# Performance work log

Hardware: AMD Instinct MI355X
Metric: run time of the kernel (lower is better)

The kernel has to match this reference:

```python
import jax, jax.numpy as jnp
import numpy as np

EPS = 1e-12  # torch.nn.functional.normalize default eps


def _l2norm(x, axis):
    n = jnp.sqrt(jnp.sum(x * x, axis=axis, keepdims=True))
    return x / jnp.maximum(n, EPS)


def setup_inputs() -> dict:
    key = jax.random.key(0)
    k1, k2 = jax.random.split(key)
    B, n_with_neg, neighbor, n_facet, emb_dim = 4096, 1, 128, 8, 16
    features = jax.random.normal(k1, (B, n_with_neg, n_facet * emb_dim), dtype=jnp.float32)
    metapath_features = jax.random.normal(
        k2, (B, n_with_neg, neighbor, n_facet * emb_dim), dtype=jnp.float32)
    return {
        "features": features,
        "metapath_features": metapath_features,
        "emb_dim": emb_dim,
        "n_facet": n_facet,
        "n_iter": 4,
    }


def reference(features, metapath_features, emb_dim, n_facet, n_iter):
    B, n = features.shape[0], features.shape[1]
    N = metapath_features.shape[2]
    # x: [B, n, F, D], z: [B, n, N, F, D]
    x = features.reshape(B, n, n_facet, emb_dim)
    z = metapath_features.reshape(B, n, N, n_facet, emb_dim)
    x = _l2norm(x, axis=3)
    z = _l2norm(z, axis=4)
    u = x
    for clus_iter in range(n_iter):
        # routing logits: dot over emb_dim -> [B, n, N, F]
        p = jnp.einsum('bnkfd,bnfd->bnkf', z, u)
        p = jax.nn.softmax(p, axis=3)
        # weighted sum over neighbors -> [B, n, F, D]
        u = jnp.einsum('bnkfd,bnkf->bnfd', z, p) + x
        if clus_iter < n_iter - 1:
            u = _l2norm(u, axis=3)
    return u.reshape(B, n_facet * emb_dim)
```

## Files before the change

### kernel.cpp

```cpp
#include <hip/hip_runtime.h>
#include <math.h>


#define CC 128

typedef unsigned u32x2 __attribute__((ext_vector_type(2)));

template<int CTRL>
__device__ __forceinline__ float dpp_add(float x) {
    int y = __builtin_amdgcn_update_dpp(0, __float_as_int(x), CTRL, 0xF, 0xF, true);
    return x + __int_as_float(y);
}
#define DPP_XOR1 0xB1
#define DPP_XOR2 0x4E
#define DPP_HMIR 0x141
#define DPP_MIR  0x140

__device__ __forceinline__ float xor16_add(float v) {
#if __has_builtin(__builtin_amdgcn_permlane16_swap)
    u32x2 r = __builtin_amdgcn_permlane16_swap(__float_as_uint(v), __float_as_uint(v), false, false);
    return __uint_as_float(r.x) + __uint_as_float(r.y);
#else
    return v + __shfl_xor(v, 16);
#endif
}
__device__ __forceinline__ float xor32_add(float v) {
#if __has_builtin(__builtin_amdgcn_permlane32_swap)
    u32x2 r = __builtin_amdgcn_permlane32_swap(__float_as_uint(v), __float_as_uint(v), false, false);
    return __uint_as_float(r.x) + __uint_as_float(r.y);
#else
    return v + __shfl_xor(v, 32);
#endif
}

__device__ __forceinline__ float rsq_guard(float s) {
    return __builtin_amdgcn_rsqf(fmaxf(s, 1e-24f));
}

__global__ __launch_bounds__(256, 4)
void hete_routing_kernel(const float* __restrict__ feat,
                         const float* __restrict__ mp,
                         float* __restrict__ out)
{
    __shared__ float part[2][4][CC];

    const int t = threadIdx.x;
    const int b = blockIdx.x;
    const int wave = t >> 6;
    const int lane = t & 63;
    const int cg = lane & 15;
    const int kgl = lane >> 4;
    const int kg = wave * 4 + kgl;
    const int c0 = cg * 8;

    const float* zg = mp + (size_t)b * (128 * CC);

    float4 za0[8], za1[8];
#pragma unroll
    for (int kk = 0; kk < 8; ++kk) {
        const float* p = zg + (kg * 8 + kk) * CC + c0;
        za0[kk] = *reinterpret_cast<const float4*>(p);
        za1[kk] = *reinterpret_cast<const float4*>(p + 4);
    }
#pragma unroll
    for (int kk = 0; kk < 8; ++kk) {
        float s = za0[kk].x * za0[kk].x + za0[kk].y * za0[kk].y
                + za0[kk].z * za0[kk].z + za0[kk].w * za0[kk].w
                + za1[kk].x * za1[kk].x + za1[kk].y * za1[kk].y
                + za1[kk].z * za1[kk].z + za1[kk].w * za1[kk].w;
        s = dpp_add<DPP_XOR1>(s);
        const float inv = rsq_guard(s);
        za0[kk].x *= inv; za0[kk].y *= inv; za0[kk].z *= inv; za0[kk].w *= inv;
        za1[kk].x *= inv; za1[kk].y *= inv; za1[kk].z *= inv; za1[kk].w *= inv;
    }

    float xr[8], ur[8];
    {
        const float* p = feat + (size_t)b * CC + c0;
        const float4 a = *reinterpret_cast<const float4*>(p);
        const float4 c = *reinterpret_cast<const float4*>(p + 4);
        xr[0] = a.x; xr[1] = a.y; xr[2] = a.z; xr[3] = a.w;
        xr[4] = c.x; xr[5] = c.y; xr[6] = c.z; xr[7] = c.w;
        float s = 0.f;
#pragma unroll
        for (int j = 0; j < 8; ++j) s += xr[j] * xr[j];
        s = dpp_add<DPP_XOR1>(s);
        const float inv = rsq_guard(s);
#pragma unroll
        for (int j = 0; j < 8; ++j) { xr[j] *= inv; ur[j] = xr[j]; }
    }

#pragma unroll
    for (int it = 0; it < 4; ++it) {
        float w[8];
#pragma unroll
        for (int kk = 0; kk < 8; ++kk) {
            float pl = za0[kk].x * ur[0] + za0[kk].y * ur[1]
                     + za0[kk].z * ur[2] + za0[kk].w * ur[3]
                     + za1[kk].x * ur[4] + za1[kk].y * ur[5]
                     + za1[kk].z * ur[6] + za1[kk].w * ur[7];
            w[kk] = dpp_add<DPP_XOR1>(pl);
        }
#pragma unroll
        for (int kk = 0; kk < 8; ++kk) {
            const float e = __expf(w[kk]);
            float su = dpp_add<DPP_XOR2>(e);
            su = dpp_add<DPP_HMIR>(su);
            su = dpp_add<DPP_MIR>(su);
            w[kk] = e * __builtin_amdgcn_rcpf(su);
        }

        float pu[8];
#pragma unroll
        for (int j = 0; j < 8; ++j) pu[j] = 0.f;
#pragma unroll
        for (int kk = 0; kk < 8; ++kk) {
            pu[0] += za0[kk].x * w[kk];
            pu[1] += za0[kk].y * w[kk];
            pu[2] += za0[kk].z * w[kk];
            pu[3] += za0[kk].w * w[kk];
            pu[4] += za1[kk].x * w[kk];
            pu[5] += za1[kk].y * w[kk];
            pu[6] += za1[kk].z * w[kk];
            pu[7] += za1[kk].w * w[kk];
        }
#pragma unroll
        for (int j = 0; j < 8; ++j) {
            pu[j] = xor16_add(pu[j]);
            pu[j] = xor32_add(pu[j]);
        }
        if (kgl == 0) {
            float* dst = &part[it & 1][wave][c0];
            *reinterpret_cast<float4*>(dst)     = make_float4(pu[0], pu[1], pu[2], pu[3]);
            *reinterpret_cast<float4*>(dst + 4) = make_float4(pu[4], pu[5], pu[6], pu[7]);
        }
        __syncthreads();

        float un[8];
#pragma unroll
        for (int j = 0; j < 8; ++j) un[j] = xr[j];
#pragma unroll
        for (int wv = 0; wv < 4; ++wv) {
            const float* src = &part[it & 1][wv][c0];
            const float4 a = *reinterpret_cast<const float4*>(src);
            const float4 c = *reinterpret_cast<const float4*>(src + 4);
            un[0] += a.x; un[1] += a.y; un[2] += a.z; un[3] += a.w;
            un[4] += c.x; un[5] += c.y; un[6] += c.z; un[7] += c.w;
        }

        if (it < 3) {
            float s = 0.f;
#pragma unroll
            for (int j = 0; j < 8; ++j) s += un[j] * un[j];
            s = dpp_add<DPP_XOR1>(s);
            const float inv = rsq_guard(s);
#pragma unroll
            for (int j = 0; j < 8; ++j) ur[j] = un[j] * inv;
        } else if (wave == 0 && kgl == 0) {
            float* dst = out + (size_t)b * CC + c0;
            *reinterpret_cast<float4*>(dst)     = make_float4(un[0], un[1], un[2], un[3]);
            *reinterpret_cast<float4*>(dst + 4) = make_float4(un[4], un[5], un[6], un[7]);
        }
    }
}

extern "C" void kernel_launch(void* const* d_in, const int* in_sizes, int n_in,
                              void* d_out, int out_size, void* d_ws, size_t ws_size,
                              hipStream_t stream) {
    const float* feat = (const float*)d_in[0];
    const float* mp   = (const float*)d_in[1];
    float* out = (float*)d_out;
    const int B = in_sizes[0] / CC;
    hete_routing_kernel<<<B, 256, 0, stream>>>(feat, mp, out);
}
```

Measured before the change: 53.28 us.

## Process eight batches per block with async global-to-LDS prefetch of next batch

Each block now handles eight consecutive batch rows instead of one. While the current row is being computed from registers, the next row's neighbor features (64 KB) stream into shared memory through global_load_lds. Each wave waits only on its own loads before pulling the prefetched tile into registers. This is meant to overlap HBM traffic with the routing math and cut per-block launch overhead, at the cost of 64 KB LDS per block, lower occupancy (launch bounds drop to 2) and a grid of only 512 blocks.

New measurement: 70.61 us. 1.33x slower.

```diff
diff --git a/kernel.cpp b/kernel.cpp
--- a/kernel.cpp
+++ b/kernel.cpp
@@ -3,6 +3,7 @@
 
 
 #define CC 128
+#define NB 8
 
 typedef unsigned u32x2 __attribute__((ext_vector_type(2)));
 
@@ -17,149 +18,182 @@
 #define DPP_MIR  0x140
 
 __device__ __forceinline__ float xor16_add(float v) {
-#if __has_builtin(__builtin_amdgcn_permlane16_swap)
     u32x2 r = __builtin_amdgcn_permlane16_swap(__float_as_uint(v), __float_as_uint(v), false, false);
     return __uint_as_float(r.x) + __uint_as_float(r.y);
-#else
-    return v + __shfl_xor(v, 16);
-#endif
 }
 __device__ __forceinline__ float xor32_add(float v) {
-#if __has_builtin(__builtin_amdgcn_permlane32_swap)
     u32x2 r = __builtin_amdgcn_permlane32_swap(__float_as_uint(v), __float_as_uint(v), false, false);
     return __uint_as_float(r.x) + __uint_as_float(r.y);
-#else
-    return v + __shfl_xor(v, 32);
-#endif
-}
-
+}
 __device__ __forceinline__ float rsq_guard(float s) {
     return __builtin_amdgcn_rsqf(fmaxf(s, 1e-24f));
 }
 
-__global__ __launch_bounds__(256, 4)
+__global__ __launch_bounds__(256, 2)
 void hete_routing_kernel(const float* __restrict__ feat,
                          const float* __restrict__ mp,
                          float* __restrict__ out)
 {
+    __shared__ float zbuf[128 * CC];
     __shared__ float part[2][4][CC];
 
     const int t = threadIdx.x;
-    const int b = blockIdx.x;
     const int wave = t >> 6;
     const int lane = t & 63;
     const int cg = lane & 15;
     const int kgl = lane >> 4;
     const int kg = wave * 4 + kgl;
     const int c0 = cg * 8;
-
-    const float* zg = mp + (size_t)b * (128 * CC);
+    const int b0 = blockIdx.x * NB;
 
     float4 za0[8], za1[8];
-#pragma unroll
-    for (int kk = 0; kk < 8; ++kk) {
-        const float* p = zg + (kg * 8 + kk) * CC + c0;
-        za0[kk] = *reinterpret_cast<const float4*>(p);
-        za1[kk] = *reinterpret_cast<const float4*>(p + 4);
+
+    {
+        const float* zg = mp + (size_t)b0 * (128 * CC);
+#pragma unroll
+        for (int kk = 0; kk < 8; ++kk) {
+            const float* p = zg + (kg * 8 + kk) * CC + c0;
+            za0[kk] = *reinterpret_cast<const float4*>(p);
+            za1[kk] = *reinterpret_cast<const float4*>(p + 4);
+        }
     }
-#pragma unroll
-    for (int kk = 0; kk < 8; ++kk) {
-        float s = za0[kk].x * za0[kk].x + za0[kk].y * za0[kk].y
-                + za0[kk].z * za0[kk].z + za0[kk].w * za0[kk].w
-                + za1[kk].x * za1[kk].x + za1[kk].y * za1[kk].y
-                + za1[kk].z * za1[kk].z + za1[kk].w * za1[kk].w;
-        s = dpp_add<DPP_XOR1>(s);
-        const float inv = rsq_guard(s);
-        za0[kk].x *= inv; za0[kk].y *= inv; za0[kk].z *= inv; za0[kk].w *= inv;
-        za1[kk].x *= inv; za1[kk].y *= inv; za1[kk].z *= inv; za1[kk].w *= inv;
+    {
+        const float* src = mp + (size_t)(b0 + 1) * (128 * CC) + wave * 4096 + lane * 4;
+        float* dst = zbuf + wave * 4096;
+#pragma unroll
+        for (int j = 0; j < 16; ++j) {
+            __builtin_amdgcn_global_load_lds(
+                (const __attribute__((address_space(1))) void*)(src + j * 256),
+                (__attribute__((address_space(3))) void*)(dst + j * 256),
+                16, 0, 0);
+        }
     }
 
-    float xr[8], ur[8];
-    {
-        const float* p = feat + (size_t)b * CC + c0;
-        const float4 a = *reinterpret_cast<const float4*>(p);
-        const float4 c = *reinterpret_cast<const float4*>(p + 4);
-        xr[0] = a.x; xr[1] = a.y; xr[2] = a.z; xr[3] = a.w;
-        xr[4] = c.x; xr[5] = c.y; xr[6] = c.z; xr[7] = c.w;
-        float s = 0.f;
-#pragma unroll
-        for (int j = 0; j < 8; ++j) s += xr[j] * xr[j];
-        s = dpp_add<DPP_XOR1>(s);
-        const float inv = rsq_guard(s);
-#pragma unroll
-        for (int j = 0; j < 8; ++j) { xr[j] *= inv; ur[j] = xr[j]; }
-    }
-
-#pragma unroll
-    for (int it = 0; it < 4; ++it) {
-        float w[8];
+#pragma unroll 1
+    for (int i = 0; i < NB; ++i) {
+        const int b = b0 + i;
+
 #pragma unroll
         for (int kk = 0; kk < 8; ++kk) {
-            float pl = za0[kk].x * ur[0] + za0[kk].y * ur[1]
-                     + za0[kk].z * ur[2] + za0[kk].w * ur[3]
-                     + za1[kk].x * ur[4] + za1[kk].y * ur[5]
-                     + za1[kk].z * ur[6] + za1[kk].w * ur[7];
-            w[kk] = dpp_add<DPP_XOR1>(pl);
-        }
-#pragma unroll
-        for (int kk = 0; kk < 8; ++kk) {
-            const float e = __expf(w[kk]);
-            float su = dpp_add<DPP_XOR2>(e);
-            su = dpp_add<DPP_HMIR>(su);
-            su = dpp_add<DPP_MIR>(su);
-            w[kk] = e * __builtin_amdgcn_rcpf(su);
-        }
-
-        float pu[8];
-#pragma unroll
-        for (int j = 0; j < 8; ++j) pu[j] = 0.f;
-#pragma unroll
-        for (int kk = 0; kk < 8; ++kk) {
-            pu[0] += za0[kk].x * w[kk];
-            pu[1] += za0[kk].y * w[kk];
-            pu[2] += za0[kk].z * w[kk];
-            pu[3] += za0[kk].w * w[kk];
-            pu[4] += za1[kk].x * w[kk];
-            pu[5] += za1[kk].y * w[kk];
-            pu[6] += za1[kk].z * w[kk];
-            pu[7] += za1[kk].w * w[kk];
-        }
-#pragma unroll
-        for (int j = 0; j < 8; ++j) {
-            pu[j] = xor16_add(pu[j]);
-            pu[j] = xor32_add(pu[j]);
-        }
-        if (kgl == 0) {
-            float* dst = &part[it & 1][wave][c0];
-            *reinterpret_cast<float4*>(dst)     = make_float4(pu[0], pu[1], pu[2], pu[3]);
-            *reinterpret_cast<float4*>(dst + 4) = make_float4(pu[4], pu[5], pu[6], pu[7]);
-        }
-        __syncthreads();
-
-        float un[8];
-#pragma unroll
-        for (int j = 0; j < 8; ++j) un[j] = xr[j];
-#pragma unroll
-        for (int wv = 0; wv < 4; ++wv) {
-            const float* src = &part[it & 1][wv][c0];
-            const float4 a = *reinterpret_cast<const float4*>(src);
-            const float4 c = *reinterpret_cast<const float4*>(src + 4);
-            un[0] += a.x; un[1] += a.y; un[2] += a.z; un[3] += a.w;
-            un[4] += c.x; un[5] += c.y; un[6] += c.z; un[7] += c.w;
-        }
-
-        if (it < 3) {
-            float s = 0.f;
-#pragma unroll
-            for (int j = 0; j < 8; ++j) s += un[j] * un[j];
+            float s = za0[kk].x * za0[kk].x + za0[kk].y * za0[kk].y
+                    + za0[kk].z * za0[kk].z + za0[kk].w * za0[kk].w
+                    + za1[kk].x * za1[kk].x + za1[kk].y * za1[kk].y
+                    + za1[kk].z * za1[kk].z + za1[kk].w * za1[kk].w;
             s = dpp_add<DPP_XOR1>(s);
             const float inv = rsq_guard(s);
-#pragma unroll
-            for (int j = 0; j < 8; ++j) ur[j] = un[j] * inv;
-        } else if (wave == 0 && kgl == 0) {
-            float* dst = out + (size_t)b * CC + c0;
-            *reinterpret_cast<float4*>(dst)     = make_float4(un[0], un[1], un[2], un[3]);
-            *reinterpret_cast<float4*>(dst + 4) = make_float4(un[4], un[5], un[6], un[7]);
+            za0[kk].x *= inv; za0[kk].y *= inv; za0[kk].z *= inv; za0[kk].w *= inv;
+            za1[kk].x *= inv; za1[kk].y *= inv; za1[kk].z *= inv; za1[kk].w *= inv;
+        }
+
+        float xr[8], ur[8];
+        {
+            const float* p = feat + (size_t)b * CC + c0;
+            const float4 a = *reinterpret_cast<const float4*>(p);
+            const float4 c = *reinterpret_cast<const float4*>(p + 4);
+            xr[0] = a.x; xr[1] = a.y; xr[2] = a.z; xr[3] = a.w;
+            xr[4] = c.x; xr[5] = c.y; xr[6] = c.z; xr[7] = c.w;
+            float s = 0.f;
+#pragma unroll
+            for (int j = 0; j < 8; ++j) s += xr[j] * xr[j];
+            s = dpp_add<DPP_XOR1>(s);
+            const float inv = rsq_guard(s);
+#pragma unroll
+            for (int j = 0; j < 8; ++j) { xr[j] *= inv; ur[j] = xr[j]; }
+        }
+
+#pragma unroll
+        for (int it = 0; it < 4; ++it) {
+            float w[8];
+#pragma unroll
+            for (int kk = 0; kk < 8; ++kk) {
+                float pl = za0[kk].x * ur[0] + za0[kk].y * ur[1]
+                         + za0[kk].z * ur[2] + za0[kk].w * ur[3]
+                         + za1[kk].x * ur[4] + za1[kk].y * ur[5]
+                         + za1[kk].z * ur[6] + za1[kk].w * ur[7];
+                w[kk] = dpp_add<DPP_XOR1>(pl);
+            }
+#pragma unroll
+            for (int kk = 0; kk < 8; ++kk) {
+                const float e = __expf(w[kk]);
+                float su = dpp_add<DPP_XOR2>(e);
+                su = dpp_add<DPP_HMIR>(su);
+                su = dpp_add<DPP_MIR>(su);
+                w[kk] = e * __builtin_amdgcn_rcpf(su);
+            }
+
+            float pu[8];
+#pragma unroll
+            for (int j = 0; j < 8; ++j) pu[j] = 0.f;
+#pragma unroll
+            for (int kk = 0; kk < 8; ++kk) {
+                pu[0] += za0[kk].x * w[kk];
+                pu[1] += za0[kk].y * w[kk];
+                pu[2] += za0[kk].z * w[kk];
+                pu[3] += za0[kk].w * w[kk];
+                pu[4] += za1[kk].x * w[kk];
+                pu[5] += za1[kk].y * w[kk];
+                pu[6] += za1[kk].z * w[kk];
+                pu[7] += za1[kk].w * w[kk];
+            }
+#pragma unroll
+            for (int j = 0; j < 8; ++j) {
+                pu[j] = xor16_add(pu[j]);
+                pu[j] = xor32_add(pu[j]);
+            }
+            if (kgl == 0) {
+                float* dst = &part[it & 1][wave][c0];
+                *reinterpret_cast<float4*>(dst)     = make_float4(pu[0], pu[1], pu[2], pu[3]);
+                *reinterpret_cast<float4*>(dst + 4) = make_float4(pu[4], pu[5], pu[6], pu[7]);
+            }
+            __syncthreads();
+
+            float un[8];
+#pragma unroll
+            for (int j = 0; j < 8; ++j) un[j] = xr[j];
+#pragma unroll
+            for (int wv = 0; wv < 4; ++wv) {
+                const float* src = &part[it & 1][wv][c0];
+                const float4 a = *reinterpret_cast<const float4*>(src);
+                const float4 c = *reinterpret_cast<const float4*>(src + 4);
+                un[0] += a.x; un[1] += a.y; un[2] += a.z; un[3] += a.w;
+                un[4] += c.x; un[5] += c.y; un[6] += c.z; un[7] += c.w;
+            }
+
+            if (it < 3) {
+                float s = 0.f;
+#pragma unroll
+                for (int j = 0; j < 8; ++j) s += un[j] * un[j];
+                s = dpp_add<DPP_XOR1>(s);
+                const float inv = rsq_guard(s);
+#pragma unroll
+                for (int j = 0; j < 8; ++j) ur[j] = un[j] * inv;
+            } else if (wave == 0 && kgl == 0) {
+                float* dst = out + (size_t)b * CC + c0;
+                *reinterpret_cast<float4*>(dst)     = make_float4(un[0], un[1], un[2], un[3]);
+                *reinterpret_cast<float4*>(dst + 4) = make_float4(un[4], un[5], un[6], un[7]);
+            }
+        }
+
+        if (i + 1 < NB) {
+            asm volatile("s_waitcnt vmcnt(0)" ::: "memory");
+#pragma unroll
+            for (int kk = 0; kk < 8; ++kk) {
+                const float* p = zbuf + (kg * 8 + kk) * CC + c0;
+                za0[kk] = *reinterpret_cast<const float4*>(p);
+                za1[kk] = *reinterpret_cast<const float4*>(p + 4);
+            }
+            asm volatile("s_waitcnt lgkmcnt(0)" ::: "memory");
+            if (i + 2 < NB) {
+                const float* src = mp + (size_t)(b0 + i + 2) * (128 * CC) + wave * 4096 + lane * 4;
+                float* dst = zbuf + wave * 4096;
+#pragma unroll
+                for (int j = 0; j < 16; ++j) {
+                    __builtin_amdgcn_global_load_lds(
+                        (const __attribute__((address_space(1))) void*)(src + j * 256),
+                        (__attribute__((address_space(3))) void*)(dst + j * 256),
+                        16, 0, 0);
+                }
+            }
         }
     }
 }
@@ -171,5 +205,5 @@
     const float* mp   = (const float*)d_in[1];
     float* out = (float*)d_out;
     const int B = in_sizes[0] / CC;
-    hete_routing_kernel<<<B, 256, 0, stream>>>(feat, mp, out);
-}
+    hete_routing_kernel<<<B / NB, 256, 0, stream>>>(feat, mp, out);
+}
```

## Process four batches per block with z prefetch and packed f32x2 math

Applied to the files above, without the earlier changes.

Each block now handles four consecutive batch rows, so the grid is a quarter of its former size. The next row's neighbor features are loaded into registers right after the final barrier of the current row, overlapping that load with the last reduction and output store. The arithmetic is rewritten on two-element float vectors so packed FMA instructions can be used, and the softmax uses exp2 with log2(e) folded into the normalization scale. The cross-wave partial-sum reduction now has each lane group read one wave's slot and then combine with lane permutes. The costs are fewer resident blocks for hiding memory latency, serialized work per block, and higher register pressure.

Measured after the change: 54.85 us. +2.9%, slower.

```diff
diff --git a/kernel.cpp b/kernel.cpp
--- a/kernel.cpp
+++ b/kernel.cpp
@@ -3,7 +3,10 @@
 
 
 #define CC 128
-
+#define NB 4
+#define LOG2E 1.44269504088896340736f
+
+typedef float f32x2 __attribute__((ext_vector_type(2)));
 typedef unsigned u32x2 __attribute__((ext_vector_type(2)));
 
 template<int CTRL>
@@ -16,25 +19,36 @@
 #define DPP_HMIR 0x141
 #define DPP_MIR  0x140
 
-__device__ __forceinline__ float xor16_add(float v) {
-#if __has_builtin(__builtin_amdgcn_permlane16_swap)
-    u32x2 r = __builtin_amdgcn_permlane16_swap(__float_as_uint(v), __float_as_uint(v), false, false);
-    return __uint_as_float(r.x) + __uint_as_float(r.y);
-#else
-    return v + __shfl_xor(v, 16);
-#endif
-}
-__device__ __forceinline__ float xor32_add(float v) {
-#if __has_builtin(__builtin_amdgcn_permlane32_swap)
-    u32x2 r = __builtin_amdgcn_permlane32_swap(__float_as_uint(v), __float_as_uint(v), false, false);
-    return __uint_as_float(r.x) + __uint_as_float(r.y);
-#else
-    return v + __shfl_xor(v, 32);
-#endif
-}
-
+__device__ __forceinline__ f32x2 xor16_add2(f32x2 v) {
+    u32x2 r0 = __builtin_amdgcn_permlane16_swap(__float_as_uint(v.x), __float_as_uint(v.x), false, false);
+    u32x2 r1 = __builtin_amdgcn_permlane16_swap(__float_as_uint(v.y), __float_as_uint(v.y), false, false);
+    f32x2 o;
+    o.x = __uint_as_float(r0.x) + __uint_as_float(r0.y);
+    o.y = __uint_as_float(r1.x) + __uint_as_float(r1.y);
+    return o;
+}
+__device__ __forceinline__ f32x2 xor32_add2(f32x2 v) {
+    u32x2 r0 = __builtin_amdgcn_permlane32_swap(__float_as_uint(v.x), __float_as_uint(v.x), false, false);
+    u32x2 r1 = __builtin_amdgcn_permlane32_swap(__float_as_uint(v.y), __float_as_uint(v.y), false, false);
+    f32x2 o;
+    o.x = __uint_as_float(r0.x) + __uint_as_float(r0.y);
+    o.y = __uint_as_float(r1.x) + __uint_as_float(r1.y);
+    return o;
+}
 __device__ __forceinline__ float rsq_guard(float s) {
     return __builtin_amdgcn_rsqf(fmaxf(s, 1e-24f));
+}
+
+__device__ __forceinline__ void load_z(f32x2 za[8][4], const float* base) {
+#pragma unroll
+    for (int kk = 0; kk < 8; ++kk) {
+        const float4 A = *reinterpret_cast<const float4*>(base + kk * CC);
+        const float4 Bv = *reinterpret_cast<const float4*>(base + kk * CC + 4);
+        za[kk][0] = f32x2{A.x, A.y};
+        za[kk][1] = f32x2{A.z, A.w};
+        za[kk][2] = f32x2{Bv.x, Bv.y};
+        za[kk][3] = f32x2{Bv.z, Bv.w};
+    }
 }
 
 __global__ __launch_bounds__(256, 4)
@@ -45,121 +59,136 @@
     __shared__ float part[2][4][CC];
 
     const int t = threadIdx.x;
-    const int b = blockIdx.x;
     const int wave = t >> 6;
     const int lane = t & 63;
     const int cg = lane & 15;
     const int kgl = lane >> 4;
     const int kg = wave * 4 + kgl;
     const int c0 = cg * 8;
-
-    const float* zg = mp + (size_t)b * (128 * CC);
-
-    float4 za0[8], za1[8];
-#pragma unroll
-    for (int kk = 0; kk < 8; ++kk) {
-        const float* p = zg + (kg * 8 + kk) * CC + c0;
-        za0[kk] = *reinterpret_cast<const float4*>(p);
-        za1[kk] = *reinterpret_cast<const float4*>(p + 4);
-    }
-#pragma unroll
-    for (int kk = 0; kk < 8; ++kk) {
-        float s = za0[kk].x * za0[kk].x + za0[kk].y * za0[kk].y
-                + za0[kk].z * za0[kk].z + za0[kk].w * za0[kk].w
-                + za1[kk].x * za1[kk].x + za1[kk].y * za1[kk].y
-                + za1[kk].z * za1[kk].z + za1[kk].w * za1[kk].w;
-        s = dpp_add<DPP_XOR1>(s);
-        const float inv = rsq_guard(s);
-        za0[kk].x *= inv; za0[kk].y *= inv; za0[kk].z *= inv; za0[kk].w *= inv;
-        za1[kk].x *= inv; za1[kk].y *= inv; za1[kk].z *= inv; za1[kk].w *= inv;
-    }
-
-    float xr[8], ur[8];
-    {
-        const float* p = feat + (size_t)b * CC + c0;
-        const float4 a = *reinterpret_cast<const float4*>(p);
-        const float4 c = *reinterpret_cast<const float4*>(p + 4);
-        xr[0] = a.x; xr[1] = a.y; xr[2] = a.z; xr[3] = a.w;
-        xr[4] = c.x; xr[5] = c.y; xr[6] = c.z; xr[7] = c.w;
-        float s = 0.f;
-#pragma unroll
-        for (int j = 0; j < 8; ++j) s += xr[j] * xr[j];
-        s = dpp_add<DPP_XOR1>(s);
-        const float inv = rsq_guard(s);
-#pragma unroll
-        for (int j = 0; j < 8; ++j) { xr[j] *= inv; ur[j] = xr[j]; }
-    }
-
-#pragma unroll
-    for (int it = 0; it < 4; ++it) {
-        float w[8];
+    const int b0 = blockIdx.x * NB;
+
+    f32x2 za[8][4];
+    const float* zb = mp + (size_t)b0 * (128 * CC) + kg * 8 * CC + c0;
+    load_z(za, zb);
+
+#pragma unroll 1
+    for (int i = 0; i < NB; ++i) {
+        const int b = b0 + i;
+
+        const float* px = feat + (size_t)b * CC + c0;
+        const float4 xa = *reinterpret_cast<const float4*>(px);
+        const float4 xc = *reinterpret_cast<const float4*>(px + 4);
+
 #pragma unroll
         for (int kk = 0; kk < 8; ++kk) {
-            float pl = za0[kk].x * ur[0] + za0[kk].y * ur[1]
-                     + za0[kk].z * ur[2] + za0[kk].w * ur[3]
-                     + za1[kk].x * ur[4] + za1[kk].y * ur[5]
-                     + za1[kk].z * ur[6] + za1[kk].w * ur[7];
-            w[kk] = dpp_add<DPP_XOR1>(pl);
-        }
-#pragma unroll
-        for (int kk = 0; kk < 8; ++kk) {
-            const float e = __expf(w[kk]);
-            float su = dpp_add<DPP_XOR2>(e);
-            su = dpp_add<DPP_HMIR>(su);
-            su = dpp_add<DPP_MIR>(su);
-            w[kk] = e * __builtin_amdgcn_rcpf(su);
-        }
-
-        float pu[8];
-#pragma unroll
-        for (int j = 0; j < 8; ++j) pu[j] = 0.f;
-#pragma unroll
-        for (int kk = 0; kk < 8; ++kk) {
-            pu[0] += za0[kk].x * w[kk];
-            pu[1] += za0[kk].y * w[kk];
-            pu[2] += za0[kk].z * w[kk];
-            pu[3] += za0[kk].w * w[kk];
-            pu[4] += za1[kk].x * w[kk];
-            pu[5] += za1[kk].y * w[kk];
-            pu[6] += za1[kk].z * w[kk];
-            pu[7] += za1[kk].w * w[kk];
-        }
-#pragma unroll
-        for (int j = 0; j < 8; ++j) {
-            pu[j] = xor16_add(pu[j]);
-            pu[j] = xor32_add(pu[j]);
-        }
-        if (kgl == 0) {
-            float* dst = &part[it & 1][wave][c0];
-            *reinterpret_cast<float4*>(dst)     = make_float4(pu[0], pu[1], pu[2], pu[3]);
-            *reinterpret_cast<float4*>(dst + 4) = make_float4(pu[4], pu[5], pu[6], pu[7]);
-        }
-        __syncthreads();
-
-        float un[8];
-#pragma unroll
-        for (int j = 0; j < 8; ++j) un[j] = xr[j];
-#pragma unroll
-        for (int wv = 0; wv < 4; ++wv) {
-            const float* src = &part[it & 1][wv][c0];
-            const float4 a = *reinterpret_cast<const float4*>(src);
-            const float4 c = *reinterpret_cast<const float4*>(src + 4);
-            un[0] += a.x; un[1] += a.y; un[2] += a.z; un[3] += a.w;
-            un[4] += c.x; un[5] += c.y; un[6] += c.z; un[7] += c.w;
-        }
-
-        if (it < 3) {
-            float s = 0.f;
-#pragma unroll
-            for (int j = 0; j < 8; ++j) s += un[j] * un[j];
+            f32x2 s2 = za[kk][0] * za[kk][0];
+            s2 += za[kk][1] * za[kk][1];
+            s2 += za[kk][2] * za[kk][2];
+            s2 += za[kk][3] * za[kk][3];
+            float s = s2.x + s2.y;
             s = dpp_add<DPP_XOR1>(s);
             const float inv = rsq_guard(s);
-#pragma unroll
-            for (int j = 0; j < 8; ++j) ur[j] = un[j] * inv;
-        } else if (wave == 0 && kgl == 0) {
-            float* dst = out + (size_t)b * CC + c0;
-            *reinterpret_cast<float4*>(dst)     = make_float4(un[0], un[1], un[2], un[3]);
-            *reinterpret_cast<float4*>(dst + 4) = make_float4(un[4], un[5], un[6], un[7]);
+            const f32x2 inv2 = {inv, inv};
+            za[kk][0] *= inv2; za[kk][1] *= inv2;
+            za[kk][2] *= inv2; za[kk][3] *= inv2;
+        }
+
+        f32x2 xr[4], ur[4];
+        {
+            xr[0] = f32x2{xa.x, xa.y}; xr[1] = f32x2{xa.z, xa.w};
+            xr[2] = f32x2{xc.x, xc.y}; xr[3] = f32x2{xc.z, xc.w};
+            f32x2 s2 = xr[0] * xr[0];
+            s2 += xr[1] * xr[1];
+            s2 += xr[2] * xr[2];
+            s2 += xr[3] * xr[3];
+            float s = s2.x + s2.y;
+            s = dpp_add<DPP_XOR1>(s);
+            const float inv = rsq_guard(s);
+            const f32x2 inv2 = {inv, inv};
+            const f32x2 invs = {inv * LOG2E, inv * LOG2E};
+#pragma unroll
+            for (int j = 0; j < 4; ++j) { ur[j] = xr[j] * invs; xr[j] *= inv2; }
+        }
+
+#pragma unroll
+        for (int it = 0; it < 4; ++it) {
+            const int p = it & 1;
+            float w[8];
+#pragma unroll
+            for (int kk = 0; kk < 8; ++kk) {
+                f32x2 acc = za[kk][0] * ur[0];
+                acc += za[kk][1] * ur[1];
+                acc += za[kk][2] * ur[2];
+                acc += za[kk][3] * ur[3];
+                w[kk] = dpp_add<DPP_XOR1>(acc.x + acc.y);
+            }
+#pragma unroll
+            for (int kk = 0; kk < 8; ++kk) {
+                const float e = __builtin_amdgcn_exp2f(w[kk]);
+                float su = dpp_add<DPP_XOR2>(e);
+                su = dpp_add<DPP_HMIR>(su);
+                su = dpp_add<DPP_MIR>(su);
+                w[kk] = e * __builtin_amdgcn_rcpf(su);
+            }
+
+            f32x2 pu[4] = {f32x2{0.f,0.f}, f32x2{0.f,0.f}, f32x2{0.f,0.f}, f32x2{0.f,0.f}};
+#pragma unroll
+            for (int kk = 0; kk < 8; ++kk) {
+                const f32x2 ws = {w[kk], w[kk]};
+                pu[0] += za[kk][0] * ws;
+                pu[1] += za[kk][1] * ws;
+                pu[2] += za[kk][2] * ws;
+                pu[3] += za[kk][3] * ws;
+            }
+#pragma unroll
+            for (int j = 0; j < 4; ++j) {
+                pu[j] = xor16_add2(pu[j]);
+                pu[j] = xor32_add2(pu[j]);
+            }
+            if (kgl == 0) {
+                float* dst = &part[p][wave][c0];
+                *reinterpret_cast<float4*>(dst)     = make_float4(pu[0].x, pu[0].y, pu[1].x, pu[1].y);
+                *reinterpret_cast<float4*>(dst + 4) = make_float4(pu[2].x, pu[2].y, pu[3].x, pu[3].y);
+            }
+            __syncthreads();
+
+            if (it == 3 && i + 1 < NB) {
+                load_z(za, zb + (size_t)(i + 1) * (128 * CC));
+            }
+
+            f32x2 pw[4];
+            {
+                const float* src = &part[p][kgl][c0];
+                const float4 A = *reinterpret_cast<const float4*>(src);
+                const float4 Cv = *reinterpret_cast<const float4*>(src + 4);
+                pw[0] = f32x2{A.x, A.y}; pw[1] = f32x2{A.z, A.w};
+                pw[2] = f32x2{Cv.x, Cv.y}; pw[3] = f32x2{Cv.z, Cv.w};
+            }
+#pragma unroll
+            for (int j = 0; j < 4; ++j) {
+                pw[j] = xor16_add2(pw[j]);
+                pw[j] = xor32_add2(pw[j]);
+            }
+            f32x2 un[4];
+#pragma unroll
+            for (int j = 0; j < 4; ++j) un[j] = xr[j] + pw[j];
+
+            if (it < 3) {
+                f32x2 s2 = un[0] * un[0];
+                s2 += un[1] * un[1];
+                s2 += un[2] * un[2];
+                s2 += un[3] * un[3];
+                float s = s2.x + s2.y;
+                s = dpp_add<DPP_XOR1>(s);
+                const float invs = rsq_guard(s) * LOG2E;
+                const f32x2 iv = {invs, invs};
+#pragma unroll
+                for (int j = 0; j < 4; ++j) ur[j] = un[j] * iv;
+            } else if (wave == 0 && kgl == 0) {
+                float* dst = out + (size_t)b * CC + c0;
+                *reinterpret_cast<float4*>(dst)     = make_float4(un[0].x, un[0].y, un[1].x, un[1].y);
+                *reinterpret_cast<float4*>(dst + 4) = make_float4(un[2].x, un[2].y, un[3].x, un[3].y);
+            }
         }
     }
 }
@@ -171,5 +200,5 @@
     const float* mp   = (const float*)d_in[1];
     float* out = (float*)d_out;
     const int B = in_sizes[0] / CC;
-    hete_routing_kernel<<<B, 256, 0, stream>>>(feat, mp, out);
-}
+    hete_routing_kernel<<<B / NB, 256, 0, stream>>>(feat, mp, out);
+}
```
